# Kernel tuning notes

Measured on AMD Instinct MI355X. Metric: run time of the kernel, lower is better.

Reference implementation:

```python
import jax, jax.numpy as jnp
import numpy as np

N_NODES = 50000
N_GRAPHS = 512
NEG_SLOPE = 0.2
EPS = 1e-16


def gat_conv(x, src, dst, W, a_src, a_dst, b):
    """PyG GATConv (heads=1, self-loops already appended, eval mode)."""
    h = x @ W                                   # [N, out]
    as_ = h @ a_src                             # [N]
    ad_ = h @ a_dst                             # [N]
    e = jax.nn.leaky_relu(as_[src] + ad_[dst], NEG_SLOPE)  # [E]
    # segment softmax over destination node
    m = jax.ops.segment_max(e, dst, num_segments=N_NODES)
    ee = jnp.exp(e - m[dst])
    s = jax.ops.segment_sum(ee, dst, num_segments=N_NODES)
    alpha = ee / (s[dst] + EPS)                 # [E]
    out = jax.ops.segment_sum(h[src] * alpha[:, None], dst, num_segments=N_NODES)
    return out + b


def setup_inputs() -> dict:
    key = jax.random.key(0)
    ks = jax.random.split(key, 16)
    vocab, d_model, hidden = 32000, 128, 128
    node_ids = jax.random.randint(ks[0], (N_NODES,), 0, vocab)
    edge_index = jax.random.randint(ks[1], (2, 800000), 0, N_NODES)
    batch = jnp.sort(jax.random.randint(ks[2], (N_NODES,), 0, N_GRAPHS))
    emb = jax.random.normal(ks[3], (vocab, d_model), jnp.float32) * 0.02

    def layer(k, din, dout):
        k1, k2, k3 = jax.random.split(k, 3)
        W = jax.random.normal(k1, (din, dout), jnp.float32) / np.sqrt(din)
        a_s = jax.random.normal(k2, (dout,), jnp.float32) / np.sqrt(dout)
        a_d = jax.random.normal(k3, (dout,), jnp.float32) / np.sqrt(dout)
        b = jnp.zeros((dout,), jnp.float32)
        return W, a_s, a_d, b

    W1, as1, ad1, b1 = layer(ks[4], d_model, hidden)
    W2, as2, ad2, b2 = layer(ks[5], hidden, hidden)
    W3, as3, ad3, b3 = layer(ks[6], hidden, hidden)
    return dict(node_ids=node_ids, edge_index=edge_index, batch=batch, emb=emb,
                W1=W1, as1=as1, ad1=ad1, b1=b1,
                W2=W2, as2=as2, ad2=ad2, b2=b2,
                W3=W3, as3=as3, ad3=ad3, b3=b3)


def reference(node_ids, edge_index, batch, emb,
              W1, as1, ad1, b1, W2, as2, ad2, b2, W3, as3, ad3, b3):
    # add self-loops (PyG GATConv default)
    loop = jnp.arange(N_NODES, dtype=edge_index.dtype)
    src = jnp.concatenate([edge_index[0], loop])
    dst = jnp.concatenate([edge_index[1], loop])

    x = emb[node_ids]                                   # [N, d_model]
    x = jax.nn.relu(gat_conv(x, src, dst, W1, as1, ad1, b1))
    x = jax.nn.relu(gat_conv(x, src, dst, W2, as2, ad2, b2))
    x = gat_conv(x, src, dst, W3, as3, ad3, b3)

    # global mean pool over graphs
    sums = jax.ops.segment_sum(x, batch, num_segments=N_GRAPHS)
    cnts = jax.ops.segment_sum(jnp.ones((N_NODES,), x.dtype), batch, num_segments=N_GRAPHS)
    return sums / jnp.maximum(cnts, 1.0)[:, None]       # [n_graphs, hidden]
```

## Files before the change

### kernel.cpp

```cpp
#include <hip/hip_runtime.h>
#include <hip/hip_fp16.h>
#include <math.h>

#define N_NODES    50000
#define N_EDGES_IN 800000
#define N_EDGES    850000
#define N_GRAPHS   512
#define NEG_SLOPE  0.2f
#define EPS_F      1e-16f

typedef _Float16 half8 __attribute__((ext_vector_type(8)));
typedef float    f32x4 __attribute__((ext_vector_type(4)));

__global__ __launch_bounds__(256) void k_gemm(const void* __restrict__ xsrc,
                                              const int* __restrict__ ids,
                                              const float* __restrict__ W,
                                              const float* __restrict__ a_s,
                                              const float* __restrict__ a_d,
                                              _Float16* __restrict__ hH,
                                              float* __restrict__ as_,
                                              float* __restrict__ ad_) {
    __shared__ _Float16 WT[128][136];
    __shared__ _Float16 Xs[128][72];
    int t = threadIdx.x;
    int row0 = blockIdx.x * 128;
    int w = t >> 6, lane = t & 63;
    int n = lane & 15, quad = lane >> 4;

    #pragma unroll
    for (int i = 0; i < 16; i++) {
        int q = t + i * 256;
        int k = q >> 5;
        int n4 = (q & 31) * 4;
        float4 v = *(const float4*)(W + (size_t)k * 128 + n4);
        WT[n4 + 0][k] = (_Float16)v.x;
        WT[n4 + 1][k] = (_Float16)v.y;
        WT[n4 + 2][k] = (_Float16)v.z;
        WT[n4 + 3][k] = (_Float16)v.w;
    }

    f32x4 acc[2][8] = {};
    for (int kc = 0; kc < 2; kc++) {
        if (kc) __syncthreads();
        if (ids == nullptr) {
            const _Float16* xH = (const _Float16*)xsrc;
            #pragma unroll
            for (int i = 0; i < 4; i++) {
                int q = t + i * 256;
                int r = q >> 3, o8 = (q & 7) * 8;
                int gr = row0 + r; if (gr >= N_NODES) gr = N_NODES - 1;
                *(half8*)&Xs[r][o8] = *(const half8*)&xH[(size_t)gr * 128 + kc * 64 + o8];
            }
        } else {
            const float* xf = (const float*)xsrc;
            #pragma unroll
            for (int i = 0; i < 4; i++) {
                int q = t + i * 256;
                int r = q >> 3, o8 = (q & 7) * 8;
                int gr = row0 + r; if (gr >= N_NODES) gr = N_NODES - 1;
                const float* src = xf + (size_t)ids[gr] * 128 + kc * 64 + o8;
                float4 v0 = *(const float4*)src;
                float4 v1 = *(const float4*)(src + 4);
                half8 hv;
                hv[0] = (_Float16)v0.x; hv[1] = (_Float16)v0.y;
                hv[2] = (_Float16)v0.z; hv[3] = (_Float16)v0.w;
                hv[4] = (_Float16)v1.x; hv[5] = (_Float16)v1.y;
                hv[6] = (_Float16)v1.z; hv[7] = (_Float16)v1.w;
                *(half8*)&Xs[r][o8] = hv;
            }
        }
        __syncthreads();
        #pragma unroll
        for (int ks = 0; ks < 2; ks++) {
            int ko = ks * 32 + quad * 8;
            half8 a0 = *(const half8*)&Xs[w * 32 + n][ko];
            half8 a1 = *(const half8*)&Xs[w * 32 + 16 + n][ko];
            int kg = kc * 64 + ko;
            #pragma unroll
            for (int c = 0; c < 8; c++) {
                half8 b = *(const half8*)&WT[c * 16 + n][kg];
                acc[0][c] = __builtin_amdgcn_mfma_f32_16x16x32_f16(a0, b, acc[0][c], 0, 0, 0);
                acc[1][c] = __builtin_amdgcn_mfma_f32_16x16x32_f16(a1, b, acc[1][c], 0, 0, 0);
            }
        }
    }

    float sa[8], da[8];
    #pragma unroll
    for (int c = 0; c < 8; c++) { sa[c] = a_s[c * 16 + n]; da[c] = a_d[c * 16 + n]; }
    #pragma unroll
    for (int r = 0; r < 2; r++) {
        float ps[4] = {0.f, 0.f, 0.f, 0.f}, pd[4] = {0.f, 0.f, 0.f, 0.f};
        #pragma unroll
        for (int reg = 0; reg < 4; reg++) {
            int row = row0 + w * 32 + r * 16 + quad * 4 + reg;
            bool ok = row < N_NODES;
            #pragma unroll
            for (int c = 0; c < 8; c++) {
                float v = acc[r][c][reg];
                ps[reg] += v * sa[c];
                pd[reg] += v * da[c];
                if (ok) hH[(size_t)row * 128 + c * 16 + n] = (_Float16)v;
            }
        }
        #pragma unroll
        for (int off = 1; off < 16; off <<= 1) {
            #pragma unroll
            for (int reg = 0; reg < 4; reg++) {
                ps[reg] += __shfl_xor(ps[reg], off, 64);
                pd[reg] += __shfl_xor(pd[reg], off, 64);
            }
        }
        if (n == 0) {
            #pragma unroll
            for (int reg = 0; reg < 4; reg++) {
                int row = row0 + w * 32 + r * 16 + quad * 4 + reg;
                if (row < N_NODES) { as_[row] = ps[reg]; ad_[row] = pd[reg]; }
            }
        }
    }
}

__global__ void k_hist(const int* __restrict__ ei, int* __restrict__ counts) {
    int e = blockIdx.x * blockDim.x + threadIdx.x;
    if (e >= N_EDGES) return;
    int d = (e < N_EDGES_IN) ? ei[N_EDGES_IN + e] : (e - N_EDGES_IN);
    atomicAdd(&counts[d], 1);
}

__global__ void k_scan1(const int* __restrict__ counts, int* __restrict__ row_ptr,
                        int* __restrict__ blksum) {
    __shared__ int s[256];
    int t = threadIdx.x, i = blockIdx.x * 256 + t;
    int v = (i < N_NODES) ? counts[i] : 0;
    s[t] = v; __syncthreads();
    for (int off = 1; off < 256; off <<= 1) {
        int x = (t >= off) ? s[t - off] : 0;
        __syncthreads(); s[t] += x; __syncthreads();
    }
    if (i < N_NODES) row_ptr[i] = s[t] - v;
    if (t == 255) blksum[blockIdx.x] = s[255];
}

__global__ void k_scan2(int* __restrict__ blksum, int nb) {
    __shared__ int s[256];
    int t = threadIdx.x;
    int v = (t < nb) ? blksum[t] : 0;
    s[t] = v; __syncthreads();
    for (int off = 1; off < 256; off <<= 1) {
        int x = (t >= off) ? s[t - off] : 0;
        __syncthreads(); s[t] += x; __syncthreads();
    }
    if (t < nb) blksum[t] = s[t] - v;
}

__global__ void k_scatter(const int* __restrict__ ei, const int* __restrict__ row_ptr,
                          const int* __restrict__ blksum,
                          int* __restrict__ fill, int* __restrict__ srcs) {
    int e = blockIdx.x * blockDim.x + threadIdx.x;
    if (e >= N_EDGES) return;
    int s, d;
    if (e < N_EDGES_IN) { s = ei[e]; d = ei[N_EDGES_IN + e]; }
    else                { s = e - N_EDGES_IN; d = s; }
    int pos = row_ptr[d] + blksum[d >> 8] + atomicAdd(&fill[d], 1);
    srcs[pos] = s;
}

__global__ __launch_bounds__(256) void k_aggregate(
        const float4* __restrict__ h16,
        const float* __restrict__ as_,
        const float* __restrict__ ad_, const int* __restrict__ row_ptr,
        const int* __restrict__ blksum,
        const int* __restrict__ srcs, const float4* __restrict__ bias4,
        float4* __restrict__ xout16,
        int do_relu) {
    int d = (blockIdx.x * blockDim.x + threadIdx.x) >> 4;
    if (d >= N_NODES) return;
    int lane = threadIdx.x & 63;
    int gl   = lane & 15;
    int base = lane & 48;
    int lo = row_ptr[d] + blksum[d >> 8];
    int hi = (d + 1 < N_NODES) ? (row_ptr[d + 1] + blksum[(d + 1) >> 8]) : N_EDGES;
    int deg = hi - lo;
    float add = ad_[d];

    float eC[4]; int sC[4];
    float m_l = -1e30f, s_l = 0.f;
    #pragma unroll
    for (int c = 0; c < 4; c++) {
        float e = -1e30f; int sidx = 0;
        int j = c * 16 + gl;
        if (j < deg) {
            sidx = srcs[lo + j];
            e = as_[sidx] + add;
            e = (e > 0.f) ? e : NEG_SLOPE * e;
            float nm = fmaxf(m_l, e);
            s_l = s_l * __expf(m_l - nm) + __expf(e - nm);
            m_l = nm;
        }
        eC[c] = e; sC[c] = sidx;
    }
    for (int j0 = 64; j0 < deg; j0 += 16) {
        int j = j0 + gl;
        if (j < deg) {
            int sidx = srcs[lo + j];
            float e = as_[sidx] + add;
            e = (e > 0.f) ? e : NEG_SLOPE * e;
            float nm = fmaxf(m_l, e);
            s_l = s_l * __expf(m_l - nm) + __expf(e - nm);
            m_l = nm;
        }
    }
    float m = m_l, s = s_l;
    #pragma unroll
    for (int off = 8; off; off >>= 1) {
        float om = __shfl_xor(m, off, 64);
        float os = __shfl_xor(s, off, 64);
        float nm = fmaxf(m, om);
        s = s * __expf(m - nm) + os * __expf(om - nm);
        m = nm;
    }
    float inv = 1.f / (s + EPS_F);

    float4 acc0 = make_float4(0.f, 0.f, 0.f, 0.f);
    float4 acc1 = make_float4(0.f, 0.f, 0.f, 0.f);
    #pragma unroll
    for (int c = 0; c < 4; c++) {
        int j0 = c * 16;
        if (j0 >= deg) break;
        float w = __expf(eC[c] - m) * inv;
        int sidx = sC[c];
        int cnt = min(16, deg - j0);
        for (int jj = 0; jj < cnt; jj += 4) {
            float w0 = __shfl(w, base + jj + 0, 64); int s0 = __shfl(sidx, base + jj + 0, 64);
            float w1 = __shfl(w, base + jj + 1, 64); int s1 = __shfl(sidx, base + jj + 1, 64);
            float w2 = __shfl(w, base + jj + 2, 64); int s2 = __shfl(sidx, base + jj + 2, 64);
            float w3 = __shfl(w, base + jj + 3, 64); int s3 = __shfl(sidx, base + jj + 3, 64);
            float4 r0 = h16[(size_t)s0 * 16 + gl];
            float4 r1 = h16[(size_t)s1 * 16 + gl];
            float4 r2 = h16[(size_t)s2 * 16 + gl];
            float4 r3 = h16[(size_t)s3 * 16 + gl];
            const __half2* p;
            float2 f0, f1, f2, f3;
            p = (const __half2*)&r0;
            f0 = __half22float2(p[0]); f1 = __half22float2(p[1]);
            f2 = __half22float2(p[2]); f3 = __half22float2(p[3]);
            acc0.x += w0*f0.x; acc0.y += w0*f0.y; acc0.z += w0*f1.x; acc0.w += w0*f1.y;
            acc1.x += w0*f2.x; acc1.y += w0*f2.y; acc1.z += w0*f3.x; acc1.w += w0*f3.y;
            p = (const __half2*)&r1;
            f0 = __half22float2(p[0]); f1 = __half22float2(p[1]);
            f2 = __half22float2(p[2]); f3 = __half22float2(p[3]);
            acc0.x += w1*f0.x; acc0.y += w1*f0.y; acc0.z += w1*f1.x; acc0.w += w1*f1.y;
            acc1.x += w1*f2.x; acc1.y += w1*f2.y; acc1.z += w1*f3.x; acc1.w += w1*f3.y;
            p = (const __half2*)&r2;
            f0 = __half22float2(p[0]); f1 = __half22float2(p[1]);
            f2 = __half22float2(p[2]); f3 = __half22float2(p[3]);
            acc0.x += w2*f0.x; acc0.y += w2*f0.y; acc0.z += w2*f1.x; acc0.w += w2*f1.y;
            acc1.x += w2*f2.x; acc1.y += w2*f2.y; acc1.z += w2*f3.x; acc1.w += w2*f3.y;
            p = (const __half2*)&r3;
            f0 = __half22float2(p[0]); f1 = __half22float2(p[1]);
            f2 = __half22float2(p[2]); f3 = __half22float2(p[3]);
            acc0.x += w3*f0.x; acc0.y += w3*f0.y; acc0.z += w3*f1.x; acc0.w += w3*f1.y;
            acc1.x += w3*f2.x; acc1.y += w3*f2.y; acc1.z += w3*f3.x; acc1.w += w3*f3.y;
        }
    }
    for (int j0 = 64; j0 < deg; j0 += 16) {
        int j = j0 + gl;
        float w = 0.f; int sidx = 0;
        if (j < deg) {
            int si = srcs[lo + j];
            float e = as_[si] + add;
            e = (e > 0.f) ? e : NEG_SLOPE * e;
            w = __expf(e - m) * inv;
            sidx = si;
        }
        int cnt = min(16, deg - j0);
        for (int jj = 0; jj < cnt; jj++) {
            float w0 = __shfl(w, base + jj, 64); int s0 = __shfl(sidx, base + jj, 64);
            float4 r0 = h16[(size_t)s0 * 16 + gl];
            const __half2* p = (const __half2*)&r0;
            float2 f0 = __half22float2(p[0]), f1 = __half22float2(p[1]);
            float2 f2 = __half22float2(p[2]), f3 = __half22float2(p[3]);
            acc0.x += w0*f0.x; acc0.y += w0*f0.y; acc0.z += w0*f1.x; acc0.w += w0*f1.y;
            acc1.x += w0*f2.x; acc1.y += w0*f2.y; acc1.z += w0*f3.x; acc1.w += w0*f3.y;
        }
    }
    float4 b0 = bias4[gl * 2], b1 = bias4[gl * 2 + 1];
    float4 o0 = make_float4(acc0.x + b0.x, acc0.y + b0.y, acc0.z + b0.z, acc0.w + b0.w);
    float4 o1 = make_float4(acc1.x + b1.x, acc1.y + b1.y, acc1.z + b1.z, acc1.w + b1.w);
    if (do_relu) {
        o0.x = fmaxf(o0.x, 0.f); o0.y = fmaxf(o0.y, 0.f);
        o0.z = fmaxf(o0.z, 0.f); o0.w = fmaxf(o0.w, 0.f);
        o1.x = fmaxf(o1.x, 0.f); o1.y = fmaxf(o1.y, 0.f);
        o1.z = fmaxf(o1.z, 0.f); o1.w = fmaxf(o1.w, 0.f);
    }
    union { __half2 h2[4]; float4 f; } pk;
    pk.h2[0] = __floats2half2_rn(o0.x, o0.y);
    pk.h2[1] = __floats2half2_rn(o0.z, o0.w);
    pk.h2[2] = __floats2half2_rn(o1.x, o1.y);
    pk.h2[3] = __floats2half2_rn(o1.z, o1.w);
    xout16[(size_t)d * 16 + gl] = pk.f;
}

__global__ __launch_bounds__(512) void k_pool(const __half* __restrict__ x,
                                              const int* __restrict__ batch,
                                              float* __restrict__ out) {
    __shared__ float red[512];
    __shared__ int sh[2];
    int g = blockIdx.x;
    int t = threadIdx.x;
    if (t == 0) {
        int lo = 0, hi = N_NODES;
        while (lo < hi) { int mid = (lo + hi) >> 1; if (batch[mid] < g) lo = mid + 1; else hi = mid; }
        sh[0] = lo;
        int lo2 = lo, hi2 = N_NODES;
        while (lo2 < hi2) { int mid = (lo2 + hi2) >> 1; if (batch[mid] < g + 1) lo2 = mid + 1; else hi2 = mid; }
        sh[1] = lo2;
    }
    __syncthreads();
    int lo = sh[0], hi = sh[1];
    int sub = t >> 7, dim = t & 127;
    float sum = 0.f;
    for (int i = lo + sub; i < hi; i += 4) sum += __half2float(x[(size_t)i * 128 + dim]);
    red[t] = sum;
    __syncthreads();
    if (t < 128) {
        float s = red[t] + red[t + 128] + red[t + 256] + red[t + 384];
        int cnt = hi - lo;
        out[g * 128 + t] = s * (cnt > 0 ? 1.f / (float)cnt : 1.f);
    }
}

extern "C" void kernel_launch(void* const* d_in, const int* in_sizes, int n_in,
                              void* d_out, int out_size, void* d_ws, size_t ws_size,
                              hipStream_t stream) {
    const int*   node_ids   = (const int*)d_in[0];
    const int*   edge_index = (const int*)d_in[1];
    const int*   batch      = (const int*)d_in[2];
    const float* emb        = (const float*)d_in[3];
    const float* W[3]  = {(const float*)d_in[4],  (const float*)d_in[8],  (const float*)d_in[12]};
    const float* As[3] = {(const float*)d_in[5],  (const float*)d_in[9],  (const float*)d_in[13]};
    const float* Ad[3] = {(const float*)d_in[6],  (const float*)d_in[10], (const float*)d_in[14]};
    const float* Bs[3] = {(const float*)d_in[7],  (const float*)d_in[11], (const float*)d_in[15]};

    char* ws = (char*)d_ws;
    size_t off = 0;
    auto alloc = [&](size_t bytes) {
        void* p = ws + off; off += (bytes + 255) & ~(size_t)255; return p;
    };
    _Float16* xH     = (_Float16*)alloc((size_t)N_NODES * 128 * 2);
    _Float16* hH     = (_Float16*)alloc((size_t)N_NODES * 128 * 2);
    float*  as_     = (float*)alloc((size_t)N_NODES * 4);
    float*  ad_     = (float*)alloc((size_t)N_NODES * 4);
    int*    counts  = (int*)alloc((size_t)N_NODES * 4);
    int*    fill    = (int*)alloc((size_t)N_NODES * 4);
    int*    row_ptr = (int*)alloc((size_t)(N_NODES + 1) * 4);
    int*    blksum  = (int*)alloc(256 * 4);
    int*    srcs    = (int*)alloc((size_t)N_EDGES * 4);
    (void)ws_size; (void)in_sizes; (void)n_in; (void)out_size;

    hipMemsetAsync(counts, 0, (size_t)((char*)row_ptr - (char*)counts), stream);

    int ebl = (N_EDGES + 255) / 256;
    int nb  = (N_NODES + 255) / 256;
    k_hist   <<<ebl, 256, 0, stream>>>(edge_index, counts);
    k_scan1  <<<nb, 256, 0, stream>>>(counts, row_ptr, blksum);
    k_scan2  <<<1, 256, 0, stream>>>(blksum, nb);
    k_scatter<<<ebl, 256, 0, stream>>>(edge_index, row_ptr, blksum, fill, srcs);

    int gemm_blocks = (N_NODES + 127) / 128;
    for (int l = 0; l < 3; l++) {
        k_gemm<<<gemm_blocks, 256, 0, stream>>>(
                 (l == 0) ? (const void*)emb : (const void*)xH,
                 (l == 0) ? node_ids : nullptr,
                 W[l], As[l], Ad[l], hH, as_, ad_);
        k_aggregate<<<(N_NODES * 16 + 255) / 256, 256, 0, stream>>>((const float4*)hH,
                 as_, ad_, row_ptr, blksum, srcs, (const float4*)Bs[l], (float4*)xH,
                 (l < 2) ? 1 : 0);
    }
    k_pool<<<N_GRAPHS, 512, 0, stream>>>((const __half*)xH, batch, (float*)d_out);
}
```

Before: 351.7 us.

## Build CSR with two-pass bucketed counting sort using shared-memory atomics

Replaces the per-edge global-atomic histogram, the two-level scan and the atomic scatter used to build the destination-sorted CSR. The new path does a coarse histogram over 256-node buckets and eight sub-slices in shared memory, scans it in one block, then scatters packed (src, local dst) records into buckets. A final per-bucket pass sorts them locally and writes both row_ptr and srcs. The goal is to cut contended global atomics and random global writes, at the cost of extra passes, an extra records buffer, and packing the source index into 16 bits, which relies on fewer than 65536 nodes.

```diff
diff --git a/kernel.cpp b/kernel.cpp
--- a/kernel.cpp
+++ b/kernel.cpp
@@ -8,6 +8,10 @@
 #define N_GRAPHS   512
 #define NEG_SLOPE  0.2f
 #define EPS_F      1e-16f
+
+#define NB_COARSE  196
+#define NSUB       8
+#define NBINS      (NB_COARSE*NSUB)
 
 typedef _Float16 half8 __attribute__((ext_vector_type(8)));
 typedef float    f32x4 __attribute__((ext_vector_type(4)));
@@ -121,66 +125,131 @@
     }
 }
 
-__global__ void k_hist(const int* __restrict__ ei, int* __restrict__ counts) {
-    int e = blockIdx.x * blockDim.x + threadIdx.x;
-    if (e >= N_EDGES) return;
-    int d = (e < N_EDGES_IN) ? ei[N_EDGES_IN + e] : (e - N_EDGES_IN);
-    atomicAdd(&counts[d], 1);
-}
-
-__global__ void k_scan1(const int* __restrict__ counts, int* __restrict__ row_ptr,
-                        int* __restrict__ blksum) {
-    __shared__ int s[256];
-    int t = threadIdx.x, i = blockIdx.x * 256 + t;
-    int v = (i < N_NODES) ? counts[i] : 0;
-    s[t] = v; __syncthreads();
+__global__ __launch_bounds__(256) void k_chist(const int* __restrict__ ei,
+                                               int* __restrict__ gbins) {
+    __shared__ int lh[NBINS];
+    for (int i = threadIdx.x; i < NBINS; i += 256) lh[i] = 0;
+    __syncthreads();
+    for (int e = blockIdx.x * 256 + threadIdx.x; e < N_EDGES; e += gridDim.x * 256) {
+        int d = (e < N_EDGES_IN) ? ei[N_EDGES_IN + e] : (e - N_EDGES_IN);
+        atomicAdd(&lh[(d >> 8) * NSUB + ((e >> 10) & 7)], 1);
+    }
+    __syncthreads();
+    for (int i = threadIdx.x; i < NBINS; i += 256) {
+        int v = lh[i];
+        if (v) atomicAdd(&gbins[i], v);
+    }
+}
+
+__global__ __launch_bounds__(256) void k_cscan(const int* __restrict__ gbins,
+                                               int* __restrict__ cbase,
+                                               int* __restrict__ row_ptr) {
+    __shared__ int part[256];
+    int t = threadIdx.x;
+    int base = t * 7;
+    int lv[7];
+    int sum = 0;
+    #pragma unroll
+    for (int i = 0; i < 7; i++) {
+        int idx = base + i;
+        int v = (idx < NBINS) ? gbins[idx] : 0;
+        lv[i] = sum; sum += v;
+    }
+    part[t] = sum; __syncthreads();
     for (int off = 1; off < 256; off <<= 1) {
-        int x = (t >= off) ? s[t - off] : 0;
-        __syncthreads(); s[t] += x; __syncthreads();
-    }
-    if (i < N_NODES) row_ptr[i] = s[t] - v;
-    if (t == 255) blksum[blockIdx.x] = s[255];
-}
-
-__global__ void k_scan2(int* __restrict__ blksum, int nb) {
-    __shared__ int s[256];
+        int x = (t >= off) ? part[t - off] : 0;
+        __syncthreads(); part[t] += x; __syncthreads();
+    }
+    int excl = part[t] - sum;
+    #pragma unroll
+    for (int i = 0; i < 7; i++) {
+        int idx = base + i;
+        if (idx < NBINS) cbase[idx] = excl + lv[i];
+    }
+    if (t == 0) { cbase[NBINS] = N_EDGES; row_ptr[N_NODES] = N_EDGES; }
+}
+
+__global__ __launch_bounds__(256) void k_scat1(const int* __restrict__ ei,
+                                               const int* __restrict__ cbase,
+                                               int* __restrict__ gcur,
+                                               int* __restrict__ recs) {
+    __shared__ int lcnt[NB_COARSE];
+    __shared__ int lbase[NB_COARSE];
     int t = threadIdx.x;
-    int v = (t < nb) ? blksum[t] : 0;
-    s[t] = v; __syncthreads();
-    for (int off = 1; off < 256; off <<= 1) {
-        int x = (t >= off) ? s[t - off] : 0;
-        __syncthreads(); s[t] += x; __syncthreads();
-    }
-    if (t < nb) blksum[t] = s[t] - v;
-}
-
-__global__ void k_scatter(const int* __restrict__ ei, const int* __restrict__ row_ptr,
-                          const int* __restrict__ blksum,
-                          int* __restrict__ fill, int* __restrict__ srcs) {
-    int e = blockIdx.x * blockDim.x + threadIdx.x;
-    if (e >= N_EDGES) return;
-    int s, d;
-    if (e < N_EDGES_IN) { s = ei[e]; d = ei[N_EDGES_IN + e]; }
-    else                { s = e - N_EDGES_IN; d = s; }
-    int pos = row_ptr[d] + blksum[d >> 8] + atomicAdd(&fill[d], 1);
-    srcs[pos] = s;
+    int e0 = blockIdx.x * 1024;
+    int sub = blockIdx.x & 7;
+    for (int i = t; i < NB_COARSE; i += 256) lcnt[i] = 0;
+    __syncthreads();
+    int s[4], d[4], b[4], r[4];
+    #pragma unroll
+    for (int i = 0; i < 4; i++) {
+        int e = e0 + t + i * 256;
+        if (e < N_EDGES) {
+            if (e < N_EDGES_IN) { s[i] = ei[e]; d[i] = ei[N_EDGES_IN + e]; }
+            else                { s[i] = e - N_EDGES_IN; d[i] = s[i]; }
+            b[i] = d[i] >> 8;
+            r[i] = atomicAdd(&lcnt[b[i]], 1);
+        } else b[i] = -1;
+    }
+    __syncthreads();
+    for (int i = t; i < NB_COARSE; i += 256) {
+        int c = lcnt[i];
+        lbase[i] = c ? (cbase[i * NSUB + sub] + atomicAdd(&gcur[i * NSUB + sub], c)) : 0;
+    }
+    __syncthreads();
+    #pragma unroll
+    for (int i = 0; i < 4; i++)
+        if (b[i] >= 0) recs[lbase[b[i]] + r[i]] = s[i] | ((d[i] & 255) << 16);
+}
+
+__global__ __launch_bounds__(256) void k_scat2(const int* __restrict__ recs,
+                                               const int* __restrict__ cbase,
+                                               int* __restrict__ row_ptr,
+                                               int* __restrict__ srcs) {
+    __shared__ int hist[256];
+    __shared__ int off[256];
+    __shared__ int rank[256];
+    int b = blockIdx.x;
+    int t = threadIdx.x;
+    int lo = cbase[b * NSUB];
+    int hi = cbase[(b + 1) * NSUB];
+    int cnt = hi - lo;
+    hist[t] = 0; rank[t] = 0;
+    __syncthreads();
+    for (int i = t; i < cnt; i += 256) atomicAdd(&hist[recs[lo + i] >> 16], 1);
+    __syncthreads();
+    int v = hist[t];
+    off[t] = v; __syncthreads();
+    for (int o = 1; o < 256; o <<= 1) {
+        int x = (t >= o) ? off[t - o] : 0;
+        __syncthreads(); off[t] += x; __syncthreads();
+    }
+    int excl = off[t] - v;
+    int dglob = b * 256 + t;
+    if (dglob < N_NODES) row_ptr[dglob] = lo + excl;
+    __syncthreads();
+    off[t] = excl;
+    __syncthreads();
+    for (int i = t; i < cnt; i += 256) {
+        int rec = recs[lo + i];
+        int dl = rec >> 16;
+        int rk = atomicAdd(&rank[dl], 1);
+        srcs[lo + off[dl] + rk] = rec & 0xFFFF;
+    }
 }
 
 __global__ __launch_bounds__(256) void k_aggregate(
         const float4* __restrict__ h16,
         const float* __restrict__ as_,
         const float* __restrict__ ad_, const int* __restrict__ row_ptr,
-        const int* __restrict__ blksum,
         const int* __restrict__ srcs, const float4* __restrict__ bias4,
-        float4* __restrict__ xout16,
-        int do_relu) {
+        float4* __restrict__ xout16, int do_relu) {
     int d = (blockIdx.x * blockDim.x + threadIdx.x) >> 4;
     if (d >= N_NODES) return;
     int lane = threadIdx.x & 63;
     int gl   = lane & 15;
     int base = lane & 48;
-    int lo = row_ptr[d] + blksum[d >> 8];
-    int hi = (d + 1 < N_NODES) ? (row_ptr[d + 1] + blksum[(d + 1) >> 8]) : N_EDGES;
+    int lo = row_ptr[d], hi = row_ptr[d + 1];
     int deg = hi - lo;
     float add = ad_[d];
 
@@ -352,21 +421,20 @@
     _Float16* hH     = (_Float16*)alloc((size_t)N_NODES * 128 * 2);
     float*  as_     = (float*)alloc((size_t)N_NODES * 4);
     float*  ad_     = (float*)alloc((size_t)N_NODES * 4);
-    int*    counts  = (int*)alloc((size_t)N_NODES * 4);
-    int*    fill    = (int*)alloc((size_t)N_NODES * 4);
+    int*    gbins   = (int*)alloc((size_t)NBINS * 4);
+    int*    gcur    = (int*)alloc((size_t)NBINS * 4);
+    int*    cbase   = (int*)alloc((size_t)(NBINS + 1) * 4);
     int*    row_ptr = (int*)alloc((size_t)(N_NODES + 1) * 4);
-    int*    blksum  = (int*)alloc(256 * 4);
+    int*    recs    = (int*)alloc((size_t)N_EDGES * 4);
     int*    srcs    = (int*)alloc((size_t)N_EDGES * 4);
     (void)ws_size; (void)in_sizes; (void)n_in; (void)out_size;
 
-    hipMemsetAsync(counts, 0, (size_t)((char*)row_ptr - (char*)counts), stream);
-
-    int ebl = (N_EDGES + 255) / 256;
-    int nb  = (N_NODES + 255) / 256;
-    k_hist   <<<ebl, 256, 0, stream>>>(edge_index, counts);
-    k_scan1  <<<nb, 256, 0, stream>>>(counts, row_ptr, blksum);
-    k_scan2  <<<1, 256, 0, stream>>>(blksum, nb);
-    k_scatter<<<ebl, 256, 0, stream>>>(edge_index, row_ptr, blksum, fill, srcs);
+    hipMemsetAsync(gbins, 0, (size_t)((char*)cbase - (char*)gbins), stream);
+
+    k_chist<<<128, 256, 0, stream>>>(edge_index, gbins);
+    k_cscan<<<1, 256, 0, stream>>>(gbins, cbase, row_ptr);
+    k_scat1<<<(N_EDGES + 1023) / 1024, 256, 0, stream>>>(edge_index, cbase, gcur, recs);
+    k_scat2<<<NB_COARSE, 256, 0, stream>>>(recs, cbase, row_ptr, srcs);
 
     int gemm_blocks = (N_NODES + 127) / 128;
     for (int l = 0; l < 3; l++) {
@@ -375,7 +443,7 @@
                  (l == 0) ? node_ids : nullptr,
                  W[l], As[l], Ad[l], hH, as_, ad_);
         k_aggregate<<<(N_NODES * 16 + 255) / 256, 256, 0, stream>>>((const float4*)hH,
-                 as_, ad_, row_ptr, blksum, srcs, (const float4*)Bs[l], (float4*)xH,
+                 as_, ad_, row_ptr, srcs, (const float4*)Bs[l], (float4*)xH,
                  (l < 2) ? 1 : 0);
     }
     k_pool<<<N_GRAPHS, 512, 0, stream>>>((const __half*)xH, batch, (float*)d_out);
```

Measured after the change: 305.4 us. 13.2% less time.
